# Kernel optimization log

Hardware: AMD Instinct MI355X
Metric: run time of the kernel (lower is better)

## Reference

```python
import jax, jax.numpy as jnp
import numpy as np

# Irreps config: node = 64x0e + 32x1o, edge sh = 1x0e + 1x1o
N, E = 50000, 800000
MUL0, MUL1 = 64, 32
D_IN = MUL0 + 3 * MUL1          # 160
FC_H = 64
W_NUMEL = MUL0 + MUL0 + MUL1 + MUL1  # 192, per-instruction uvu weights
SQRT3 = 1.7320508075688772
ACT_C = 1.6791   # e3nn normalize2mom constant for silu


def setup_inputs() -> dict:
    key = jax.random.key(0)
    ks = jax.random.split(key, 11)
    return {
        "x": jax.random.normal(ks[0], (N, D_IN), jnp.float32),
        "edge_scalars": jax.random.uniform(ks[1], (E, FC_H), dtype=jnp.float32),
        "edge_attr_sh": jax.random.normal(ks[2], (E, 4), jnp.float32),
        "edge_index": jax.random.randint(ks[3], (2, E), 0, N),
        "w_fc1": jax.random.normal(ks[4], (FC_H, FC_H), jnp.float32),
        "w_fc2": jax.random.normal(ks[5], (FC_H, W_NUMEL), jnp.float32),
        "w_sc_s": jax.random.normal(ks[6], (MUL0, MUL0), jnp.float32),
        "w_sc_v": jax.random.normal(ks[7], (MUL1, MUL1), jnp.float32),
        "w_lin_s": jax.random.normal(ks[8], (96, MUL0), jnp.float32),
        "w_lin_v": jax.random.normal(ks[9], (96, MUL1), jnp.float32),
        "w_alpha": jax.random.normal(ks[10], (96, 1), jnp.float32) * 0.1,
    }


def reference(x, edge_scalars, edge_attr_sh, edge_index, w_fc1, w_fc2,
              w_sc_s, w_sc_v, w_lin_s, w_lin_v, w_alpha):
    src, dst = edge_index[0], edge_index[1]

    # --- fc: FullyConnectedNet([64, 64, 192], silu), e3nn fan-in norm ---
    h = jax.nn.silu(edge_scalars @ w_fc1 / np.sqrt(FC_H)) * ACT_C
    weight = h @ w_fc2 / np.sqrt(FC_H)                       # [E, 192]
    w0 = weight[:, :MUL0]                 # 0e x 0e -> 0e (mul 64)
    w1 = weight[:, MUL0:2 * MUL0]         # 0e x 1o -> 1o (mul 64)
    w2 = weight[:, 2 * MUL0:2 * MUL0 + MUL1]   # 1o x 0e -> 1o (mul 32)
    w3 = weight[:, 2 * MUL0 + MUL1:]           # 1o x 1o -> 0e (mul 32)

    # --- self connection: o3.Linear(in -> out), per-irrep mixing ---
    x_s = x[:, :MUL0]                                   # [N, 64]
    x_v = x[:, MUL0:].reshape(N, MUL1, 3)               # [N, 32, 3]
    sc_s = x_s @ w_sc_s / np.sqrt(MUL0)
    sc_v = jnp.einsum('nui,uw->nwi', x_v, w_sc_v) / np.sqrt(MUL1)
    sc_out = jnp.concatenate([sc_s, sc_v.reshape(N, 3 * MUL1)], axis=1)

    # --- gather + edge-weighted uvu tensor product ---
    gx_s = x_s[src]                                     # [E, 64]
    gx_v = x_v[src]                                     # [E, 32, 3]
    sh_s = edge_attr_sh[:, 0:1]                         # [E, 1]
    sh_v = edge_attr_sh[:, 1:4]                         # [E, 3]

    # path weights fold with w3j so factors cancel for 1o outputs
    mid_s0 = w0 * gx_s * sh_s                                        # [E,64] 0e
    mid_s1 = w3 * jnp.einsum('eui,ei->eu', gx_v, sh_v) / SQRT3       # [E,32] 0e
    mid_v0 = w1[:, :, None] * gx_s[:, :, None] * sh_v[:, None, :]    # [E,64,3] 1o
    mid_v1 = w2[:, :, None] * gx_v * sh_s[:, :, None]                # [E,32,3] 1o
    edge_feat = jnp.concatenate(
        [mid_s0, mid_s1, mid_v0.reshape(E, 3 * MUL0), mid_v1.reshape(E, 3 * MUL1)],
        axis=1)                                                      # [E, 384]

    # --- scatter-mean to destination nodes ---
    seg = jax.ops.segment_sum(edge_feat, dst, num_segments=N)
    cnt = jax.ops.segment_sum(jnp.ones((E,), edge_feat.dtype), dst, num_segments=N)
    mean = seg / jnp.maximum(cnt, 1.0)[:, None]                      # [N, 384]

    m_s = mean[:, :96]                                   # 96x0e
    m_v = mean[:, 96:].reshape(N, 96, 3)                 # 96x1o

    # --- alpha gate (o3.Linear mid -> 0e) and output linear ---
    alpha = m_s @ w_alpha / np.sqrt(96)                  # [N, 1]
    lin_s = m_s @ w_lin_s / np.sqrt(96)                  # [N, 64]
    lin_v = jnp.einsum('nui,uw->nwi', m_v, w_lin_v) / np.sqrt(96)
    lin_out = jnp.concatenate([lin_s, lin_v.reshape(N, 3 * MUL1)], axis=1)

    # sc.output_mask is all-ones here (every output irrep reachable)
    return sc_out + alpha * lin_out
```

## Files before the change

kernel.cpp:

```cpp
#include <hip/hip_runtime.h>
#include <hip/hip_bf16.h>

#define N_NODES 50000
#define N_EDGES 800000
#define MUL0 64
#define MUL1 32
#define D_IN 160
#define FC_H 64
#define W_NUMEL 192
#define FEAT 384
#define ACT_C 1.6791f
#define INV_SQRT3 0.57735026918962576f
#define RSQRT32 0.17677669529663687f
#define RSQRT96 0.10206207261596575f

#define TILE 64
#define NWG_EDGE (N_EDGES / TILE)

typedef __attribute__((ext_vector_type(8))) short s16x8;
typedef __attribute__((ext_vector_type(4))) float f32x4;
typedef _Float16 h8 __attribute__((ext_vector_type(8)));
typedef __fp16 fp16x2 __attribute__((ext_vector_type(2)));

static __device__ __forceinline__ unsigned short f2bf(float f) {
    __hip_bfloat16 b = __float2bfloat16(f);
    return __builtin_bit_cast(unsigned short, b);
}

static __device__ __forceinline__ int swz(int row, int byte_in_row) {
    int unit = ((row & 1) << 2) | (byte_in_row >> 4);
    int su = unit ^ ((row >> 1) & 7);
    return (row >> 1) * 128 + su * 16 + (byte_in_row & 15);
}
static __device__ __forceinline__ h8 rdh8(const unsigned char* base, int row, int eb) {
    return *(const h8*)(base + swz(row, eb));
}


#define HIST_NB ((N_EDGES + 255) / 256)

__global__ __launch_bounds__(256) void hist_prep_kernel(
    const int*   __restrict__ eidx,
    int*         __restrict__ cnt,
    const float* __restrict__ w_fc1,
    const float* __restrict__ w_fc2,
    const float* __restrict__ w_sc_s,
    const float* __restrict__ w_sc_v,
    const float* __restrict__ w_lin_s,
    const float* __restrict__ w_lin_v,
    unsigned short* __restrict__ w1t,
    unsigned short* __restrict__ w2t,
    unsigned short* __restrict__ wscs_t,
    unsigned short* __restrict__ wscv_t,
    unsigned short* __restrict__ wlins_t,
    unsigned short* __restrict__ wlinv_t)
{
    int b = blockIdx.x;
    if (b < HIST_NB) {
        int e = b * 256 + threadIdx.x;
        if (e < N_EDGES) atomicAdd(&cnt[eidx[N_EDGES + e]], 1);
    } else {
        int i = (b - HIST_NB) * 256 + threadIdx.x;
        if (i < 64 * 64)  w1t[i]    = f2bf(w_fc1[(i & 63) * FC_H + (i >> 6)]);
        if (i < 192 * 64) w2t[i]    = f2bf(w_fc2[(i & 63) * W_NUMEL + (i >> 6)]);
        if (i < 64 * 64)  wscs_t[i] = f2bf(w_sc_s[(i & 63) * 64 + (i >> 6)]);
        if (i < 32 * 32)  wscv_t[i] = f2bf(w_sc_v[(i & 31) * 32 + (i >> 5)]);
        if (i < 64 * 96)  wlins_t[i] = f2bf(w_lin_s[(i % 96) * 64 + (i / 96)]);
        if (i < 32 * 96)  wlinv_t[i] = f2bf(w_lin_v[(i % 96) * 32 + (i / 96)]);
    }
}

#define SCAN_NB 64
#define SCAN_CH ((N_NODES + SCAN_NB - 1) / SCAN_NB)

__global__ __launch_bounds__(256) void scanA_kernel(const int* __restrict__ cnt,
                                                    int* __restrict__ bsum) {
    __shared__ int sred[4];
    int b = blockIdx.x, t = threadIdx.x;
    int lim = min((b + 1) * SCAN_CH, N_NODES);
    int s = 0;
    for (int i = b * SCAN_CH + t; i < lim; i += 256) s += cnt[i];
    for (int d = 1; d < 64; d <<= 1) s += __shfl_xor(s, d);
    if ((t & 63) == 0) sred[t >> 6] = s;
    __syncthreads();
    if (t == 0) bsum[b] = sred[0] + sred[1] + sred[2] + sred[3];
}

__global__ __launch_bounds__(256) void scanC_kernel(const int* __restrict__ cnt,
                                                    const int* __restrict__ bsum,
                                                    int* __restrict__ fill) {
    __shared__ int s_w[4];
    __shared__ int s_boff;
    int b = blockIdx.x, t = threadIdx.x;
    if (t < 64) {
        int v = bsum[t];
        int p = v;
        for (int d = 1; d < 64; d <<= 1) { int u = __shfl_up(p, d); if (t >= d) p += u; }
        if (t == b) s_boff = p - v;
    }
    const int CH2 = (SCAN_CH + 255) / 256;
    int base = b * SCAN_CH + t * CH2;
    int lim = min((b + 1) * SCAN_CH, N_NODES);
    int s = 0;
#pragma unroll
    for (int k = 0; k < CH2; ++k) { int i = base + k; if (i < lim) s += cnt[i]; }
    int v = s;
    for (int d = 1; d < 64; d <<= 1) { int u = __shfl_up(v, d); if ((t & 63) >= d) v += u; }
    if ((t & 63) == 63) s_w[t >> 6] = v;
    __syncthreads();
    if (t == 0) { int run = 0; for (int w = 0; w < 4; ++w) { int tv = s_w[w]; s_w[w] = run; run += tv; } }
    __syncthreads();
    int run = s_boff + s_w[t >> 6] + (v - s);
#pragma unroll
    for (int k = 0; k < CH2; ++k) {
        int i = base + k;
        if (i < lim) { fill[i] = run; run += cnt[i]; }
    }
}

__global__ __launch_bounds__(256) void scatter_ids_kernel(const int* __restrict__ eidx,
                                                          int* __restrict__ fill,
                                                          int* __restrict__ sorted_eid,
                                                          int* __restrict__ sorted_src,
                                                          int* __restrict__ sorted_dst) {
    int e = blockIdx.x * 256 + threadIdx.x;
    if (e < N_EDGES) {
        int d = eidx[N_EDGES + e];
        int s = eidx[e];
        int p = atomicAdd(&fill[d], 1);
        sorted_eid[p] = e;
        sorted_src[p] = s;
        sorted_dst[p] = d;
    }
}

#define X_OFF    0
#define W_OFF    20480
#define SH_OFF   45056
#define SID_OFF  45568
#define SEGN_OFF 45696
#define NSEG_OFF 45952
#define SMEM_SZ  45968

static __device__ __forceinline__ h8 seg_mask(const unsigned* vv, unsigned tgt) {
    h8 a;
#pragma unroll
    for (int w2 = 0; w2 < 4; ++w2) {
        a[w2 * 2]     = ((vv[w2] & 0xffffu) == tgt) ? (_Float16)1.f : (_Float16)0.f;
        a[w2 * 2 + 1] = ((vv[w2] >> 16)     == tgt) ? (_Float16)1.f : (_Float16)0.f;
    }
    return a;
}

__global__ __launch_bounds__(256) void edge_kernel(
    const float* __restrict__ x,
    const float* __restrict__ es,
    const float* __restrict__ sh,
    const int*   __restrict__ sorted_eid,
    const int*   __restrict__ sorted_src,
    const int*   __restrict__ sorted_dst,
    const unsigned short* __restrict__ w1t,
    const unsigned short* __restrict__ w2t,
    float* __restrict__ accg)
{
    __shared__ __align__(16) unsigned char smem[SMEM_SZ];
    int* s_segnode = (int*)(smem + SEGN_OFF);
    unsigned short* s_sid = (unsigned short*)(smem + SID_OFF);

    const int t = threadIdx.x;
    const int l = t & 63;
    const int wv = t >> 6;
    const int lr = l & 15;
    const int lk = l >> 4;
    int bid;
    {
        const int nwg = NWG_EDGE;
        int orig = blockIdx.x;
        int xcd = orig & 7, idx = orig >> 3;
        int q = nwg >> 3, r = nwg & 7;
        bid = (xcd < r ? xcd * (q + 1) : r * (q + 1) + (xcd - r) * q) + idx;
    }
    const int tile0 = bid * TILE;

    int eid_own = sorted_eid[tile0 + wv * 16 + lr];
    float4 esf[4];
    {
        const float4* ep = (const float4*)(es + (size_t)eid_own * FC_H);
        esf[0] = ep[lk * 2];     esf[1] = ep[lk * 2 + 1];
        esf[2] = ep[8 + lk * 2]; esf[3] = ep[8 + lk * 2 + 1];
    }
    const int hs   = t >> 7;
    const int tt_h = t & 127;
    const int xe   = tt_h & 31;
    const int cgrp = tt_h >> 5;
    float4 xg[10];
    {
        const float4* xp = (const float4*)(x + (size_t)sorted_src[tile0 + hs * 32 + xe] * D_IN);
#pragma unroll
        for (int k = 0; k < 10; ++k) xg[k] = xp[cgrp * 10 + k];
    }
    float shv = sh[(size_t)sorted_eid[tile0 + (t >> 2)] * 4 + (t & 3)];
    if (wv == 0) {
        int dl = sorted_dst[tile0 + l];
        int nd = __shfl_down(dl, 1);
        bool flag = (l == 63) || (dl != nd);
        unsigned long long m = __ballot(flag);
        int sid = __popcll(m & ((1ull << l) - 1ull));
        s_sid[l] = (unsigned short)sid;
        if (flag) s_segnode[sid] = dl;
        if (l == 63) *(int*)(smem + NSEG_OFF) = sid + 1;
    }

    unsigned short* s_h = (unsigned short*)(smem + X_OFF);
    s16x8 afrag[2];
    {
        s16x8 a;
        a[0] = f2bf(esf[0].x); a[1] = f2bf(esf[0].y); a[2] = f2bf(esf[0].z); a[3] = f2bf(esf[0].w);
        a[4] = f2bf(esf[1].x); a[5] = f2bf(esf[1].y); a[6] = f2bf(esf[1].z); a[7] = f2bf(esf[1].w);
        afrag[0] = a;
        a[0] = f2bf(esf[2].x); a[1] = f2bf(esf[2].y); a[2] = f2bf(esf[2].z); a[3] = f2bf(esf[2].w);
        a[4] = f2bf(esf[3].x); a[5] = f2bf(esf[3].y); a[6] = f2bf(esf[3].z); a[7] = f2bf(esf[3].w);
        afrag[1] = a;
    }
#pragma unroll
    for (int nt = 0; nt < 4; ++nt) {
        f32x4 hacc = {0.f, 0.f, 0.f, 0.f};
#pragma unroll
        for (int kk = 0; kk < 2; ++kk) {
            s16x8 b = *(const s16x8*)(w1t + (nt * 16 + lr) * 64 + kk * 32 + lk * 8);
            hacc = __builtin_amdgcn_mfma_f32_16x16x32_bf16(afrag[kk], b, hacc, 0, 0, 0);
        }
#pragma unroll
        for (int q = 0; q < 4; ++q) {
            float aa = hacc[q] * 0.125f;
            float hv = aa * (1.f / (1.f + __expf(-aa))) * ACT_C;
            s_h[(wv * 16 + lk * 4 + q) * 72 + nt * 16 + lr] = f2bf(hv);
        }
    }
    s16x8 hfrag[2];
#pragma unroll
    for (int kk = 0; kk < 2; ++kk)
        hfrag[kk] = *(const s16x8*)(s_h + (wv * 16 + lr) * 72 + kk * 32 + lk * 8);
    __syncthreads();

    {
        const int ws = wv >> 1;
        const int ebyte = (wv & 1) * 32 + lk * 8;
        unsigned char* bw = smem + W_OFF + ws * 12288;
#pragma unroll
        for (int nt = 0; nt < 12; ++nt) {
            f32x4 acc = {0.f, 0.f, 0.f, 0.f};
#pragma unroll
            for (int kk = 0; kk < 2; ++kk) {
                s16x8 b = *(const s16x8*)(w2t + (nt * 16 + lr) * 64 + kk * 32 + lk * 8);
                acc = __builtin_amdgcn_mfma_f32_16x16x32_bf16(hfrag[kk], b, acc, 0, 0, 0);
            }
            int f = nt * 16 + lr;
            fp16x2 p0 = __builtin_amdgcn_cvt_pkrtz(acc[0] * 0.125f, acc[1] * 0.125f);
            fp16x2 p1 = __builtin_amdgcn_cvt_pkrtz(acc[2] * 0.125f, acc[3] * 0.125f);
            uint2 wval = { __builtin_bit_cast(unsigned, p0), __builtin_bit_cast(unsigned, p1) };
            *(uint2*)(bw + swz(f, ebyte)) = wval;
        }
    }
    {
        unsigned char* bx = smem + X_OFF + hs * 10240;
#pragma unroll
        for (int k = 0; k < 10; ++k) {
            float4 v = xg[k];
#pragma unroll
            for (int jj = 0; jj < 4; ++jj) {
                int r = (cgrp * 10 + k) * 4 + jj;
                float fv = (jj == 0) ? v.x : (jj == 1) ? v.y : (jj == 2) ? v.z : v.w;
                *(_Float16*)(bx + swz(r, xe * 2)) = (_Float16)fv;
            }
        }
    }
    {
        int e = t >> 2, c = t & 3;
        *(_Float16*)(smem + SH_OFF + (e >> 5) * 256 + swz(c, (e & 31) * 2)) = (_Float16)shv;
    }
    __syncthreads();

    const int nseg = *(const int*)(smem + NSEG_OFF);
    const int eb = lk * 16;

    h8 shreg[4][2];
    unsigned vv[2][4];
#pragma unroll
    for (int ks = 0; ks < 2; ++ks) {
#pragma unroll
        for (int r = 0; r < 4; ++r)
            shreg[r][ks] = rdh8(smem + SH_OFF + ks * 256, r, eb);
        uint4 sv = *(const uint4*)(smem + SID_OFF + ks * 64 + lk * 16);
        vv[ks][0] = sv.x; vv[ks][1] = sv.y; vv[ks][2] = sv.z; vv[ks][3] = sv.w;
    }

    h8 Bv[4][2];
    int fcol[4];
    bool cls3j[4] = {false, false, false, false};
#pragma unroll
    for (int ks = 0; ks < 2; ++ks) {
        const unsigned char* bx = smem + X_OFF + ks * 10240;
        const unsigned char* bw = smem + W_OFF + ks * 12288;
        if (wv == 0) {
#pragma unroll
            for (int jj = 0; jj < 4; ++jj) {
                int col = jj * 16 + lr;
                Bv[jj][ks] = rdh8(bw, col, eb) * rdh8(bx, col, eb);
                fcol[jj] = col;
            }
        } else if (wv == 1) {
#pragma unroll
            for (int jj = 0; jj < 4; ++jj) {
                int col = jj * 16 + lr;
                Bv[jj][ks] = rdh8(bw, 128 + col / 3, eb) * rdh8(bx, 64 + col, eb);
                fcol[jj] = 288 + col;
            }
        } else if (wv == 2) {
#pragma unroll
            for (int jj = 0; jj < 2; ++jj) {
                int col = 64 + jj * 16 + lr;
                Bv[jj][ks] = rdh8(bw, 128 + col / 3, eb) * rdh8(bx, 64 + col, eb);
                fcol[jj] = 288 + col;
            }
#pragma unroll
            for (int jj = 2; jj < 4; ++jj) {
                int col = (jj - 2) * 16 + lr;
                h8 d = rdh8(bx, 64 + 3 * col, eb)     * shreg[1][ks]
                     + rdh8(bx, 64 + 3 * col + 1, eb) * shreg[2][ks]
                     + rdh8(bx, 64 + 3 * col + 2, eb) * shreg[3][ks];
                Bv[jj][ks] = rdh8(bw, 160 + col, eb) * d;
                fcol[jj] = 64 + col;
                cls3j[jj] = true;
            }
        } else {
#pragma unroll
            for (int jj = 0; jj < 4; ++jj) {
                int col = jj * 16 + lr;
                Bv[jj][ks] = rdh8(bw, 64 + col, eb) * rdh8(bx, col, eb);
                fcol[jj] = 96 + 3 * col;
            }
        }
    }

    if (wv != 3) {
        const int npass = (nseg + 15) >> 4;
        for (int p = 0; p < npass; ++p) {
            h8 bm0 = seg_mask(vv[0], (unsigned)(p * 16 + lr));
            h8 bm1 = seg_mask(vv[1], (unsigned)(p * 16 + lr));
            h8 As0 = bm0 * shreg[0][0];
            h8 As1 = bm1 * shreg[0][1];
            const int m0 = p * 16 + lk * 4;
            float* nptr[4]; bool valid[4], atq[4];
#pragma unroll
            for (int q = 0; q < 4; ++q) {
                int sg = m0 + q;
                valid[q] = sg < nseg;
                int node = valid[q] ? s_segnode[sg] : 0;
                nptr[q] = accg + (size_t)node * FEAT;
                atq[q] = (sg == 0) || (sg == nseg - 1);
            }
#pragma unroll
            for (int jj = 0; jj < 4; ++jj) {
                f32x4 acc = {0.f, 0.f, 0.f, 0.f};
                acc = __builtin_amdgcn_mfma_f32_16x16x32_f16(cls3j[jj] ? bm0 : As0, Bv[jj][0], acc, 0, 0, 0);
                acc = __builtin_amdgcn_mfma_f32_16x16x32_f16(cls3j[jj] ? bm1 : As1, Bv[jj][1], acc, 0, 0, 0);
                const float sc = cls3j[jj] ? INV_SQRT3 : 1.f;
#pragma unroll
                for (int q = 0; q < 4; ++q) {
                    if (valid[q]) {
                        float v = acc[q] * sc;
                        float* a = nptr[q] + fcol[jj];
                        if (atq[q]) atomicAdd(a, v); else *a = v;
                    }
                }
            }
        }
    } else {
        const int npass = (3 * nseg + 15) >> 4;
        for (int p = 0; p < npass; ++p) {
            int m = p * 16 + lr;
            int sgA = m / 3, i3A = m - 3 * sgA;
            h8 mk0 = seg_mask(vv[0], (unsigned)sgA);
            h8 mk1 = seg_mask(vv[1], (unsigned)sgA);
            h8 A0 = mk0 * ((i3A == 0) ? shreg[1][0] : (i3A == 1) ? shreg[2][0] : shreg[3][0]);
            h8 A1 = mk1 * ((i3A == 0) ? shreg[1][1] : (i3A == 1) ? shreg[2][1] : shreg[3][1]);
            int m0 = p * 16 + lk * 4;
            int sgq = m0 / 3, rq = m0 - 3 * sgq;
            float* nptr[4]; int i3q[4]; bool valid[4], atq[4];
#pragma unroll
            for (int q = 0; q < 4; ++q) {
                valid[q] = sgq < nseg;
                int node = valid[q] ? s_segnode[sgq] : 0;
                nptr[q] = accg + (size_t)node * FEAT;
                i3q[q] = rq;
                atq[q] = (sgq == 0) || (sgq == nseg - 1);
                if (++rq == 3) { rq = 0; ++sgq; }
            }
#pragma unroll
            for (int jj = 0; jj < 4; ++jj) {
                f32x4 acc = {0.f, 0.f, 0.f, 0.f};
                acc = __builtin_amdgcn_mfma_f32_16x16x32_f16(A0, Bv[jj][0], acc, 0, 0, 0);
                acc = __builtin_amdgcn_mfma_f32_16x16x32_f16(A1, Bv[jj][1], acc, 0, 0, 0);
#pragma unroll
                for (int q = 0; q < 4; ++q) {
                    if (valid[q]) {
                        float* a = nptr[q] + fcol[jj] + i3q[q];
                        if (atq[q]) atomicAdd(a, acc[q]); else *a = acc[q];
                    }
                }
            }
        }
    }
}


static __device__ __forceinline__ s16x8 frag_c8(const float* p, float s) {
    float4 u = *(const float4*)p, v = *(const float4*)(p + 4);
    s16x8 a;
    a[0] = f2bf(u.x * s); a[1] = f2bf(u.y * s); a[2] = f2bf(u.z * s); a[3] = f2bf(u.w * s);
    a[4] = f2bf(v.x * s); a[5] = f2bf(v.y * s); a[6] = f2bf(v.z * s); a[7] = f2bf(v.w * s);
    return a;
}

__global__ __launch_bounds__(256) void node_kernel(
    const float* __restrict__ x,
    const float* __restrict__ accg,
    const int*   __restrict__ cnt,
    const unsigned short* __restrict__ wscs_t,
    const unsigned short* __restrict__ wscv_t,
    const unsigned short* __restrict__ wlins_t,
    const unsigned short* __restrict__ wlinv_t,
    const float* __restrict__ w_alpha,
    float* __restrict__ out)
{
    const int t = threadIdx.x;
    const int wv = t >> 6, l = t & 63;
    const int lr = l & 15, lk = l >> 4;
    const int n_base = blockIdx.x * 64 + wv * 16;
    const int nrow = n_base + lr;
    const int nclamp = min(nrow, N_NODES - 1);

    const float* mrow = accg + (size_t)nclamp * FEAT;
    const float* xrow = x + (size_t)nclamp * D_IN;
    const float rinv = 1.f / (float)max(cnt[nclamp], 1);

    s16x8 ax[2], ams[3], axv[3], amv[3][3];
#pragma unroll
    for (int kk = 0; kk < 2; ++kk) ax[kk] = frag_c8(xrow + kk * 32 + lk * 8, 1.f);
#pragma unroll
    for (int kk = 0; kk < 3; ++kk) ams[kk] = frag_c8(mrow + kk * 32 + lk * 8, rinv);
    {
        float xb[24];
        const float4* p = (const float4*)(xrow + 64 + 24 * lk);
#pragma unroll
        for (int q = 0; q < 6; ++q) ((float4*)xb)[q] = p[q];
#pragma unroll
        for (int i = 0; i < 3; ++i) {
            s16x8 a;
#pragma unroll
            for (int j = 0; j < 8; ++j) a[j] = f2bf(xb[3 * j + i]);
            axv[i] = a;
        }
    }
#pragma unroll
    for (int kk = 0; kk < 3; ++kk) {
        float mb[24];
        const float4* p = (const float4*)(mrow + 96 + 96 * kk + 24 * lk);
#pragma unroll
        for (int q = 0; q < 6; ++q) ((float4*)mb)[q] = p[q];
#pragma unroll
        for (int i = 0; i < 3; ++i) {
            s16x8 a;
#pragma unroll
            for (int j = 0; j < 8; ++j) a[j] = f2bf(mb[3 * j + i] * rinv);
            amv[i][kk] = a;
        }
    }

    float ap = 0.f;
    {
        float ab[24];
        const float4* p = (const float4*)(mrow + 24 * lk);
#pragma unroll
        for (int q = 0; q < 6; ++q) ((float4*)ab)[q] = p[q];
#pragma unroll
        for (int j = 0; j < 24; ++j) ap += ab[j] * rinv * w_alpha[lk * 24 + j];
    }
    ap += __shfl_xor(ap, 16);
    ap += __shfl_xor(ap, 32);
    const float alphav = ap * RSQRT96;

    f32x4 accA[4], accL[4];
#pragma unroll
    for (int nt = 0; nt < 4; ++nt) { accA[nt] = (f32x4){0,0,0,0}; accL[nt] = (f32x4){0,0,0,0}; }
#pragma unroll
    for (int nt = 0; nt < 4; ++nt) {
#pragma unroll
        for (int kk = 0; kk < 2; ++kk) {
            s16x8 b = *(const s16x8*)(wscs_t + (nt * 16 + lr) * 64 + kk * 32 + lk * 8);
            accA[nt] = __builtin_amdgcn_mfma_f32_16x16x32_bf16(ax[kk], b, accA[nt], 0, 0, 0);
        }
#pragma unroll
        for (int kk = 0; kk < 3; ++kk) {
            s16x8 b = *(const s16x8*)(wlins_t + (nt * 16 + lr) * 96 + kk * 32 + lk * 8);
            accL[nt] = __builtin_amdgcn_mfma_f32_16x16x32_bf16(ams[kk], b, accL[nt], 0, 0, 0);
        }
    }
    f32x4 accVs[3][2], accVl[3][2];
#pragma unroll
    for (int i = 0; i < 3; ++i)
#pragma unroll
        for (int nt = 0; nt < 2; ++nt) { accVs[i][nt] = (f32x4){0,0,0,0}; accVl[i][nt] = (f32x4){0,0,0,0}; }
#pragma unroll
    for (int i = 0; i < 3; ++i) {
#pragma unroll
        for (int nt = 0; nt < 2; ++nt) {
            s16x8 b = *(const s16x8*)(wscv_t + (nt * 16 + lr) * 32 + lk * 8);
            accVs[i][nt] = __builtin_amdgcn_mfma_f32_16x16x32_bf16(axv[i], b, accVs[i][nt], 0, 0, 0);
#pragma unroll
            for (int kk = 0; kk < 3; ++kk) {
                s16x8 b2 = *(const s16x8*)(wlinv_t + (nt * 16 + lr) * 96 + kk * 32 + lk * 8);
                accVl[i][nt] = __builtin_amdgcn_mfma_f32_16x16x32_bf16(amv[i][kk], b2, accVl[i][nt], 0, 0, 0);
            }
        }
    }

#pragma unroll
    for (int q = 0; q < 4; ++q) {
        int row = lk * 4 + q;
        float ar = __shfl(alphav, row);
        int n = n_base + row;
        bool ok = (n < N_NODES);
        float* orow = out + (size_t)n * 160;
#pragma unroll
        for (int nt = 0; nt < 4; ++nt) {
            float vout = accA[nt][q] * 0.125f + ar * accL[nt][q] * RSQRT96;
            if (ok) orow[nt * 16 + lr] = vout;
        }
#pragma unroll
        for (int i = 0; i < 3; ++i)
#pragma unroll
            for (int nt = 0; nt < 2; ++nt) {
                float vout = accVs[i][nt][q] * RSQRT32 + ar * accVl[i][nt][q] * RSQRT96;
                if (ok) orow[64 + 3 * (nt * 16 + lr) + i] = vout;
            }
    }
}


extern "C" void kernel_launch(void* const* d_in, const int* in_sizes, int n_in,
                              void* d_out, int out_size, void* d_ws, size_t ws_size,
                              hipStream_t stream) {
    const float* x        = (const float*)d_in[0];
    const float* es       = (const float*)d_in[1];
    const float* sh       = (const float*)d_in[2];
    const int*   eidx     = (const int*)d_in[3];
    const float* w_fc1    = (const float*)d_in[4];
    const float* w_fc2    = (const float*)d_in[5];
    const float* w_sc_s   = (const float*)d_in[6];
    const float* w_sc_v   = (const float*)d_in[7];
    const float* w_lin_s  = (const float*)d_in[8];
    const float* w_lin_v  = (const float*)d_in[9];
    const float* w_alpha  = (const float*)d_in[10];
    float* out = (float*)d_out;

    float* accg       = (float*)d_ws;
    int*   cnt        = (int*)(accg + (size_t)N_NODES * FEAT);
    int*   fill       = cnt + N_NODES;
    int*   sorted_eid = fill + N_NODES;
    int*   sorted_src = sorted_eid + N_EDGES;
    int*   sorted_dst = sorted_src + N_EDGES;
    unsigned short* w1t     = (unsigned short*)(sorted_dst + N_EDGES);
    unsigned short* w2t     = w1t + 64 * 64;
    unsigned short* wscs_t  = w2t + 192 * 64;
    unsigned short* wscv_t  = wscs_t + 64 * 64;
    unsigned short* wlins_t = wscv_t + 32 * 32;
    unsigned short* wlinv_t = wlins_t + 64 * 96;
    int* bsum = (int*)(wlinv_t + 32 * 96);

    (void)hipMemsetAsync(d_ws, 0, ((size_t)N_NODES * FEAT + N_NODES) * 4, stream);
    hipLaunchKernelGGL(hist_prep_kernel, dim3(HIST_NB + 48), dim3(256), 0, stream,
                       eidx, cnt, w_fc1, w_fc2, w_sc_s, w_sc_v, w_lin_s, w_lin_v,
                       w1t, w2t, wscs_t, wscv_t, wlins_t, wlinv_t);
    hipLaunchKernelGGL(scanA_kernel, dim3(SCAN_NB), dim3(256), 0, stream, cnt, bsum);
    hipLaunchKernelGGL(scanC_kernel, dim3(SCAN_NB), dim3(256), 0, stream, cnt, bsum, fill);
    hipLaunchKernelGGL(scatter_ids_kernel, dim3((N_EDGES + 255) / 256), dim3(256), 0, stream,
                       eidx, fill, sorted_eid, sorted_src, sorted_dst);
    hipLaunchKernelGGL(edge_kernel, dim3(NWG_EDGE), dim3(256), 0, stream,
                       x, es, sh, sorted_eid, sorted_src, sorted_dst, w1t, w2t, accg);
    hipLaunchKernelGGL(node_kernel, dim3((N_NODES + 63) / 64), dim3(256), 0, stream,
                       x, accg, cnt, wscs_t, wscv_t, wlins_t, wlinv_t, w_alpha, out);
}
```

Baseline: 453.5 us.

## Split fused edge kernel into MLP weight kernel and scatter kernel

Measured after the change: 548.1 us. +20.9%, slower.

```diff
diff --git a/kernel.cpp b/kernel.cpp
--- a/kernel.cpp
+++ b/kernel.cpp
@@ -16,11 +16,14 @@
 
 #define TILE 64
 #define NWG_EDGE (N_EDGES / TILE)
+#define WT_TILE_BYTES 24576
 
 typedef __attribute__((ext_vector_type(8))) short s16x8;
 typedef __attribute__((ext_vector_type(4))) float f32x4;
 typedef _Float16 h8 __attribute__((ext_vector_type(8)));
 typedef __fp16 fp16x2 __attribute__((ext_vector_type(2)));
+typedef __attribute__((address_space(1))) const void gv_t;
+typedef __attribute__((address_space(3))) void lv_t;
 
 static __device__ __forceinline__ unsigned short f2bf(float f) {
     __hip_bfloat16 b = __float2bfloat16(f);
@@ -134,6 +137,79 @@
     }
 }
 
+
+__global__ __launch_bounds__(256) void mlp_kernel(
+    const float* __restrict__ es,
+    const int*   __restrict__ sorted_eid,
+    const unsigned short* __restrict__ w1t,
+    const unsigned short* __restrict__ w2t,
+    unsigned char* __restrict__ wsT)
+{
+    __shared__ unsigned short s_h[64 * 72];
+
+    const int t = threadIdx.x;
+    const int l = t & 63;
+    const int wv = t >> 6;
+    const int lr = l & 15;
+    const int lk = l >> 4;
+    const int tile0 = blockIdx.x * TILE;
+
+    int eid_own = sorted_eid[tile0 + wv * 16 + lr];
+    float4 esf[4];
+    {
+        const float4* ep = (const float4*)(es + (size_t)eid_own * FC_H);
+        esf[0] = ep[lk * 2];     esf[1] = ep[lk * 2 + 1];
+        esf[2] = ep[8 + lk * 2]; esf[3] = ep[8 + lk * 2 + 1];
+    }
+
+    s16x8 afrag[2];
+    {
+        s16x8 a;
+        a[0] = f2bf(esf[0].x); a[1] = f2bf(esf[0].y); a[2] = f2bf(esf[0].z); a[3] = f2bf(esf[0].w);
+        a[4] = f2bf(esf[1].x); a[5] = f2bf(esf[1].y); a[6] = f2bf(esf[1].z); a[7] = f2bf(esf[1].w);
+        afrag[0] = a;
+        a[0] = f2bf(esf[2].x); a[1] = f2bf(esf[2].y); a[2] = f2bf(esf[2].z); a[3] = f2bf(esf[2].w);
+        a[4] = f2bf(esf[3].x); a[5] = f2bf(esf[3].y); a[6] = f2bf(esf[3].z); a[7] = f2bf(esf[3].w);
+        afrag[1] = a;
+    }
+#pragma unroll
+    for (int nt = 0; nt < 4; ++nt) {
+        f32x4 hacc = {0.f, 0.f, 0.f, 0.f};
+#pragma unroll
+        for (int kk = 0; kk < 2; ++kk) {
+            s16x8 b = *(const s16x8*)(w1t + (nt * 16 + lr) * 64 + kk * 32 + lk * 8);
+            hacc = __builtin_amdgcn_mfma_f32_16x16x32_bf16(afrag[kk], b, hacc, 0, 0, 0);
+        }
+#pragma unroll
+        for (int q = 0; q < 4; ++q) {
+            float aa = hacc[q] * 0.125f;
+            float hv = aa * (1.f / (1.f + __expf(-aa))) * ACT_C;
+            s_h[(wv * 16 + lk * 4 + q) * 72 + nt * 16 + lr] = f2bf(hv);
+        }
+    }
+    s16x8 hfrag[2];
+#pragma unroll
+    for (int kk = 0; kk < 2; ++kk)
+        hfrag[kk] = *(const s16x8*)(s_h + (wv * 16 + lr) * 72 + kk * 32 + lk * 8);
+
+    unsigned char* bw = wsT + (size_t)blockIdx.x * WT_TILE_BYTES + (wv >> 1) * 12288;
+    const int ebyte = (wv & 1) * 32 + lk * 8;
+#pragma unroll
+    for (int nt = 0; nt < 12; ++nt) {
+        f32x4 acc = {0.f, 0.f, 0.f, 0.f};
+#pragma unroll
+        for (int kk = 0; kk < 2; ++kk) {
+            s16x8 b = *(const s16x8*)(w2t + (nt * 16 + lr) * 64 + kk * 32 + lk * 8);
+            acc = __builtin_amdgcn_mfma_f32_16x16x32_bf16(hfrag[kk], b, acc, 0, 0, 0);
+        }
+        int f = nt * 16 + lr;
+        fp16x2 p0 = __builtin_amdgcn_cvt_pkrtz(acc[0] * 0.125f, acc[1] * 0.125f);
+        fp16x2 p1 = __builtin_amdgcn_cvt_pkrtz(acc[2] * 0.125f, acc[3] * 0.125f);
+        uint2 wval = { __builtin_bit_cast(unsigned, p0), __builtin_bit_cast(unsigned, p1) };
+        *(uint2*)(bw + swz(f, ebyte)) = wval;
+    }
+}
+
 #define X_OFF    0
 #define W_OFF    20480
 #define SH_OFF   45056
@@ -151,6 +227,227 @@
     }
     return a;
 }
+
+static __device__ __forceinline__ void phase_c(
+    unsigned char* smem, int wv, int lr, int lk, float* __restrict__ accg)
+{
+    int* s_segnode = (int*)(smem + SEGN_OFF);
+    const int nseg = *(const int*)(smem + NSEG_OFF);
+    const int eb = lk * 16;
+
+    h8 shreg[4][2];
+    unsigned vv[2][4];
+#pragma unroll
+    for (int ks = 0; ks < 2; ++ks) {
+#pragma unroll
+        for (int r = 0; r < 4; ++r)
+            shreg[r][ks] = rdh8(smem + SH_OFF + ks * 256, r, eb);
+        uint4 sv = *(const uint4*)(smem + SID_OFF + ks * 64 + lk * 16);
+        vv[ks][0] = sv.x; vv[ks][1] = sv.y; vv[ks][2] = sv.z; vv[ks][3] = sv.w;
+    }
+
+    h8 Bv[4][2];
+    int fcol[4];
+    bool cls3j[4] = {false, false, false, false};
+#pragma unroll
+    for (int ks = 0; ks < 2; ++ks) {
+        const unsigned char* bx = smem + X_OFF + ks * 10240;
+        const unsigned char* bw = smem + W_OFF + ks * 12288;
+        if (wv == 0) {
+#pragma unroll
+            for (int jj = 0; jj < 4; ++jj) {
+                int col = jj * 16 + lr;
+                Bv[jj][ks] = rdh8(bw, col, eb) * rdh8(bx, col, eb);
+                fcol[jj] = col;
+            }
+        } else if (wv == 1) {
+#pragma unroll
+            for (int jj = 0; jj < 4; ++jj) {
+                int col = jj * 16 + lr;
+                Bv[jj][ks] = rdh8(bw, 128 + col / 3, eb) * rdh8(bx, 64 + col, eb);
+                fcol[jj] = 288 + col;
+            }
+        } else if (wv == 2) {
+#pragma unroll
+            for (int jj = 0; jj < 2; ++jj) {
+                int col = 64 + jj * 16 + lr;
+                Bv[jj][ks] = rdh8(bw, 128 + col / 3, eb) * rdh8(bx, 64 + col, eb);
+                fcol[jj] = 288 + col;
+            }
+#pragma unroll
+            for (int jj = 2; jj < 4; ++jj) {
+                int col = (jj - 2) * 16 + lr;
+                h8 d = rdh8(bx, 64 + 3 * col, eb)     * shreg[1][ks]
+                     + rdh8(bx, 64 + 3 * col + 1, eb) * shreg[2][ks]
+                     + rdh8(bx, 64 + 3 * col + 2, eb) * shreg[3][ks];
+                Bv[jj][ks] = rdh8(bw, 160 + col, eb) * d;
+                fcol[jj] = 64 + col;
+                cls3j[jj] = true;
+            }
+        } else {
+#pragma unroll
+            for (int jj = 0; jj < 4; ++jj) {
+                int col = jj * 16 + lr;
+                Bv[jj][ks] = rdh8(bw, 64 + col, eb) * rdh8(bx, col, eb);
+                fcol[jj] = 96 + 3 * col;
+            }
+        }
+    }
+
+    if (wv != 3) {
+        const int npass = (nseg + 15) >> 4;
+        for (int p = 0; p < npass; ++p) {
+            h8 bm0 = seg_mask(vv[0], (unsigned)(p * 16 + lr));
+            h8 bm1 = seg_mask(vv[1], (unsigned)(p * 16 + lr));
+            h8 As0 = bm0 * shreg[0][0];
+            h8 As1 = bm1 * shreg[0][1];
+            const int m0 = p * 16 + lk * 4;
+            float* nptr[4]; bool valid[4], atq[4];
+#pragma unroll
+            for (int q = 0; q < 4; ++q) {
+                int sg = m0 + q;
+                valid[q] = sg < nseg;
+                int node = valid[q] ? s_segnode[sg] : 0;
+                nptr[q] = accg + (size_t)node * FEAT;
+                atq[q] = (sg == 0) || (sg == nseg - 1);
+            }
+#pragma unroll
+            for (int jj = 0; jj < 4; ++jj) {
+                f32x4 acc = {0.f, 0.f, 0.f, 0.f};
+                acc = __builtin_amdgcn_mfma_f32_16x16x32_f16(cls3j[jj] ? bm0 : As0, Bv[jj][0], acc, 0, 0, 0);
+                acc = __builtin_amdgcn_mfma_f32_16x16x32_f16(cls3j[jj] ? bm1 : As1, Bv[jj][1], acc, 0, 0, 0);
+                const float sc = cls3j[jj] ? INV_SQRT3 : 1.f;
+#pragma unroll
+                for (int q = 0; q < 4; ++q) {
+                    if (valid[q]) {
+                        float v = acc[q] * sc;
+                        float* a = nptr[q] + fcol[jj];
+                        if (atq[q]) atomicAdd(a, v); else *a = v;
+                    }
+                }
+            }
+        }
+    } else {
+        const int npass = (3 * nseg + 15) >> 4;
+        for (int p = 0; p < npass; ++p) {
+            int m = p * 16 + lr;
+            int sgA = m / 3, i3A = m - 3 * sgA;
+            h8 mk0 = seg_mask(vv[0], (unsigned)sgA);
+            h8 mk1 = seg_mask(vv[1], (unsigned)sgA);
+            h8 A0 = mk0 * ((i3A == 0) ? shreg[1][0] : (i3A == 1) ? shreg[2][0] : shreg[3][0]);
+            h8 A1 = mk1 * ((i3A == 0) ? shreg[1][1] : (i3A == 1) ? shreg[2][1] : shreg[3][1]);
+            int m0 = p * 16 + lk * 4;
+            int sgq = m0 / 3, rq = m0 - 3 * sgq;
+            float* nptr[4]; int i3q[4]; bool valid[4], atq[4];
+#pragma unroll
+            for (int q = 0; q < 4; ++q) {
+                valid[q] = sgq < nseg;
+                int node = valid[q] ? s_segnode[sgq] : 0;
+                nptr[q] = accg + (size_t)node * FEAT;
+                i3q[q] = rq;
+                atq[q] = (sgq == 0) || (sgq == nseg - 1);
+                if (++rq == 3) { rq = 0; ++sgq; }
+            }
+#pragma unroll
+            for (int jj = 0; jj < 4; ++jj) {
+                f32x4 acc = {0.f, 0.f, 0.f, 0.f};
+                acc = __builtin_amdgcn_mfma_f32_16x16x32_f16(A0, Bv[jj][0], acc, 0, 0, 0);
+                acc = __builtin_amdgcn_mfma_f32_16x16x32_f16(A1, Bv[jj][1], acc, 0, 0, 0);
+#pragma unroll
+                for (int q = 0; q < 4; ++q) {
+                    if (valid[q]) {
+                        float* a = nptr[q] + fcol[jj] + i3q[q];
+                        if (atq[q]) atomicAdd(a, acc[q]); else *a = acc[q];
+                    }
+                }
+            }
+        }
+    }
+}
+
+
+__global__ __launch_bounds__(256) void scatter_kernel(
+    const float* __restrict__ x,
+    const float* __restrict__ sh,
+    const int*   __restrict__ sorted_eid,
+    const int*   __restrict__ sorted_src,
+    const int*   __restrict__ sorted_dst,
+    const unsigned char* __restrict__ wsT,
+    float* __restrict__ accg)
+{
+    __shared__ __align__(16) unsigned char smem[SMEM_SZ];
+    int* s_segnode = (int*)(smem + SEGN_OFF);
+    unsigned short* s_sid = (unsigned short*)(smem + SID_OFF);
+
+    const int t = threadIdx.x;
+    const int l = t & 63;
+    const int wv = t >> 6;
+    const int lr = l & 15;
+    const int lk = l >> 4;
+    int bid;
+    {
+        const int nwg = NWG_EDGE;
+        int orig = blockIdx.x;
+        int xcd = orig & 7, idx = orig >> 3;
+        int q = nwg >> 3, r = nwg & 7;
+        bid = (xcd < r ? xcd * (q + 1) : r * (q + 1) + (xcd - r) * q) + idx;
+    }
+    const int tile0 = bid * TILE;
+
+    {
+        const unsigned char* gsrc = wsT + (size_t)bid * WT_TILE_BYTES;
+#pragma unroll
+        for (int i = 0; i < 6; ++i) {
+            __builtin_amdgcn_global_load_lds(
+                (gv_t*)(gsrc + i * 4096 + wv * 1024 + l * 16),
+                (lv_t*)(smem + W_OFF + i * 4096 + wv * 1024), 16, 0, 0);
+        }
+    }
+
+    const int hs   = t >> 7;
+    const int tt_h = t & 127;
+    const int xe   = tt_h & 31;
+    const int cgrp = tt_h >> 5;
+    float4 xg[10];
+    {
+        const float4* xp = (const float4*)(x + (size_t)sorted_src[tile0 + hs * 32 + xe] * D_IN);
+#pragma unroll
+        for (int k = 0; k < 10; ++k) xg[k] = xp[cgrp * 10 + k];
+    }
+    float shv = sh[(size_t)sorted_eid[tile0 + (t >> 2)] * 4 + (t & 3)];
+    if (wv == 0) {
+        int dl = sorted_dst[tile0 + l];
+        int nd = __shfl_down(dl, 1);
+        bool flag = (l == 63) || (dl != nd);
+        unsigned long long m = __ballot(flag);
+        int sid = __popcll(m & ((1ull << l) - 1ull));
+        s_sid[l] = (unsigned short)sid;
+        if (flag) s_segnode[sid] = dl;
+        if (l == 63) *(int*)(smem + NSEG_OFF) = sid + 1;
+    }
+
+    {
+        unsigned char* bx = smem + X_OFF + hs * 10240;
+#pragma unroll
+        for (int k = 0; k < 10; ++k) {
+            float4 v = xg[k];
+#pragma unroll
+            for (int jj = 0; jj < 4; ++jj) {
+                int r = (cgrp * 10 + k) * 4 + jj;
+                float fv = (jj == 0) ? v.x : (jj == 1) ? v.y : (jj == 2) ? v.z : v.w;
+                *(_Float16*)(bx + swz(r, xe * 2)) = (_Float16)fv;
+            }
+        }
+    }
+    {
+        int e = t >> 2, c = t & 3;
+        *(_Float16*)(smem + SH_OFF + (e >> 5) * 256 + swz(c, (e & 31) * 2)) = (_Float16)shv;
+    }
+    __syncthreads();
+
+    phase_c(smem, wv, lr, lk, accg);
+}
+
 
 __global__ __launch_bounds__(256) void edge_kernel(
     const float* __restrict__ x,
@@ -281,137 +578,7 @@
     }
     __syncthreads();
 
-    const int nseg = *(const int*)(smem + NSEG_OFF);
-    const int eb = lk * 16;
-
-    h8 shreg[4][2];
-    unsigned vv[2][4];
-#pragma unroll
-    for (int ks = 0; ks < 2; ++ks) {
-#pragma unroll
-        for (int r = 0; r < 4; ++r)
-            shreg[r][ks] = rdh8(smem + SH_OFF + ks * 256, r, eb);
-        uint4 sv = *(const uint4*)(smem + SID_OFF + ks * 64 + lk * 16);
-        vv[ks][0] = sv.x; vv[ks][1] = sv.y; vv[ks][2] = sv.z; vv[ks][3] = sv.w;
-    }
-
-    h8 Bv[4][2];
-    int fcol[4];
-    bool cls3j[4] = {false, false, false, false};
-#pragma unroll
-    for (int ks = 0; ks < 2; ++ks) {
-        const unsigned char* bx = smem + X_OFF + ks * 10240;
-        const unsigned char* bw = smem + W_OFF + ks * 12288;
-        if (wv == 0) {
-#pragma unroll
-            for (int jj = 0; jj < 4; ++jj) {
-                int col = jj * 16 + lr;
-                Bv[jj][ks] = rdh8(bw, col, eb) * rdh8(bx, col, eb);
-                fcol[jj] = col;
-            }
-        } else if (wv == 1) {
-#pragma unroll
-            for (int jj = 0; jj < 4; ++jj) {
-                int col = jj * 16 + lr;
-                Bv[jj][ks] = rdh8(bw, 128 + col / 3, eb) * rdh8(bx, 64 + col, eb);
-                fcol[jj] = 288 + col;
-            }
-        } else if (wv == 2) {
-#pragma unroll
-            for (int jj = 0; jj < 2; ++jj) {
-                int col = 64 + jj * 16 + lr;
-                Bv[jj][ks] = rdh8(bw, 128 + col / 3, eb) * rdh8(bx, 64 + col, eb);
-                fcol[jj] = 288 + col;
-            }
-#pragma unroll
-            for (int jj = 2; jj < 4; ++jj) {
-                int col = (jj - 2) * 16 + lr;
-                h8 d = rdh8(bx, 64 + 3 * col, eb)     * shreg[1][ks]
-                     + rdh8(bx, 64 + 3 * col + 1, eb) * shreg[2][ks]
-                     + rdh8(bx, 64 + 3 * col + 2, eb) * shreg[3][ks];
-                Bv[jj][ks] = rdh8(bw, 160 + col, eb) * d;
-                fcol[jj] = 64 + col;
-                cls3j[jj] = true;
-            }
-        } else {
-#pragma unroll
-            for (int jj = 0; jj < 4; ++jj) {
-                int col = jj * 16 + lr;
-                Bv[jj][ks] = rdh8(bw, 64 + col, eb) * rdh8(bx, col, eb);
-                fcol[jj] = 96 + 3 * col;
-            }
-        }
-    }
-
-    if (wv != 3) {
-        const int npass = (nseg + 15) >> 4;
-        for (int p = 0; p < npass; ++p) {
-            h8 bm0 = seg_mask(vv[0], (unsigned)(p * 16 + lr));
-            h8 bm1 = seg_mask(vv[1], (unsigned)(p * 16 + lr));
-            h8 As0 = bm0 * shreg[0][0];
-            h8 As1 = bm1 * shreg[0][1];
-            const int m0 = p * 16 + lk * 4;
-            float* nptr[4]; bool valid[4], atq[4];
-#pragma unroll
-            for (int q = 0; q < 4; ++q) {
-                int sg = m0 + q;
-                valid[q] = sg < nseg;
-                int node = valid[q] ? s_segnode[sg] : 0;
-                nptr[q] = accg + (size_t)node * FEAT;
-                atq[q] = (sg == 0) || (sg == nseg - 1);
-            }
-#pragma unroll
-            for (int jj = 0; jj < 4; ++jj) {
-                f32x4 acc = {0.f, 0.f, 0.f, 0.f};
-                acc = __builtin_amdgcn_mfma_f32_16x16x32_f16(cls3j[jj] ? bm0 : As0, Bv[jj][0], acc, 0, 0, 0);
-                acc = __builtin_amdgcn_mfma_f32_16x16x32_f16(cls3j[jj] ? bm1 : As1, Bv[jj][1], acc, 0, 0, 0);
-                const float sc = cls3j[jj] ? INV_SQRT3 : 1.f;
-#pragma unroll
-                for (int q = 0; q < 4; ++q) {
-                    if (valid[q]) {
-                        float v = acc[q] * sc;
-                        float* a = nptr[q] + fcol[jj];
-                        if (atq[q]) atomicAdd(a, v); else *a = v;
-                    }
-                }
-            }
-        }
-    } else {
-        const int npass = (3 * nseg + 15) >> 4;
-        for (int p = 0; p < npass; ++p) {
-            int m = p * 16 + lr;
-            int sgA = m / 3, i3A = m - 3 * sgA;
-            h8 mk0 = seg_mask(vv[0], (unsigned)sgA);
-            h8 mk1 = seg_mask(vv[1], (unsigned)sgA);
-            h8 A0 = mk0 * ((i3A == 0) ? shreg[1][0] : (i3A == 1) ? shreg[2][0] : shreg[3][0]);
-            h8 A1 = mk1 * ((i3A == 0) ? shreg[1][1] : (i3A == 1) ? shreg[2][1] : shreg[3][1]);
-            int m0 = p * 16 + lk * 4;
-            int sgq = m0 / 3, rq = m0 - 3 * sgq;
-            float* nptr[4]; int i3q[4]; bool valid[4], atq[4];
-#pragma unroll
-            for (int q = 0; q < 4; ++q) {
-                valid[q] = sgq < nseg;
-                int node = valid[q] ? s_segnode[sgq] : 0;
-                nptr[q] = accg + (size_t)node * FEAT;
-                i3q[q] = rq;
-                atq[q] = (sgq == 0) || (sgq == nseg - 1);
-                if (++rq == 3) { rq = 0; ++sgq; }
-            }
-#pragma unroll
-            for (int jj = 0; jj < 4; ++jj) {
-                f32x4 acc = {0.f, 0.f, 0.f, 0.f};
-                acc = __builtin_amdgcn_mfma_f32_16x16x32_f16(A0, Bv[jj][0], acc, 0, 0, 0);
-                acc = __builtin_amdgcn_mfma_f32_16x16x32_f16(A1, Bv[jj][1], acc, 0, 0, 0);
-#pragma unroll
-                for (int q = 0; q < 4; ++q) {
-                    if (valid[q]) {
-                        float* a = nptr[q] + fcol[jj] + i3q[q];
-                        if (atq[q]) atomicAdd(a, acc[q]); else *a = acc[q];
-                    }
-                }
-            }
-        }
-    }
+    phase_c(smem, wv, lr, lk, accg);
 }
 
 
@@ -578,6 +745,11 @@
     unsigned short* wlins_t = wscv_t + 32 * 32;
     unsigned short* wlinv_t = wlins_t + 64 * 96;
     int* bsum = (int*)(wlinv_t + 32 * 96);
+    size_t base_bytes = (size_t)((unsigned char*)(bsum + SCAN_NB) - (unsigned char*)d_ws);
+    base_bytes = (base_bytes + 15) & ~(size_t)15;
+    unsigned char* wsT = (unsigned char*)d_ws + base_bytes;
+    size_t needed = base_bytes + (size_t)NWG_EDGE * WT_TILE_BYTES;
+    const bool use_split = (ws_size >= needed);
 
     (void)hipMemsetAsync(d_ws, 0, ((size_t)N_NODES * FEAT + N_NODES) * 4, stream);
     hipLaunchKernelGGL(hist_prep_kernel, dim3(HIST_NB + 48), dim3(256), 0, stream,
@@ -587,8 +759,15 @@
     hipLaunchKernelGGL(scanC_kernel, dim3(SCAN_NB), dim3(256), 0, stream, cnt, bsum, fill);
     hipLaunchKernelGGL(scatter_ids_kernel, dim3((N_EDGES + 255) / 256), dim3(256), 0, stream,
                        eidx, fill, sorted_eid, sorted_src, sorted_dst);
-    hipLaunchKernelGGL(edge_kernel, dim3(NWG_EDGE), dim3(256), 0, stream,
-                       x, es, sh, sorted_eid, sorted_src, sorted_dst, w1t, w2t, accg);
+    if (use_split) {
+        hipLaunchKernelGGL(mlp_kernel, dim3(NWG_EDGE), dim3(256), 0, stream,
+                           es, sorted_eid, w1t, w2t, wsT);
+        hipLaunchKernelGGL(scatter_kernel, dim3(NWG_EDGE), dim3(256), 0, stream,
+                           x, sh, sorted_eid, sorted_src, sorted_dst, wsT, accg);
+    } else {
+        hipLaunchKernelGGL(edge_kernel, dim3(NWG_EDGE), dim3(256), 0, stream,
+                           x, es, sh, sorted_eid, sorted_src, sorted_dst, w1t, w2t, accg);
+    }
     hipLaunchKernelGGL(node_kernel, dim3((N_NODES + 63) / 64), dim3(256), 0, stream,
                        x, accg, cnt, wscs_t, wscv_t, wlins_t, wlinv_t, w_alpha, out);
 }
```

## Pre-permute edge scalars to bf16 and sh into sorted order during scatter

Applied to the files above, without the earlier changes.

New measurement: 517.7 us. +14.1%, slower.

```diff
diff --git a/kernel.cpp b/kernel.cpp
--- a/kernel.cpp
+++ b/kernel.cpp
@@ -118,19 +118,32 @@
     }
 }
 
-__global__ __launch_bounds__(256) void scatter_ids_kernel(const int* __restrict__ eidx,
-                                                          int* __restrict__ fill,
-                                                          int* __restrict__ sorted_eid,
-                                                          int* __restrict__ sorted_src,
-                                                          int* __restrict__ sorted_dst) {
+__global__ __launch_bounds__(256) void scatter_ids_kernel(
+    const int*   __restrict__ eidx,
+    const float* __restrict__ es,
+    const float* __restrict__ sh,
+    int* __restrict__ fill,
+    int* __restrict__ sorted_src,
+    int* __restrict__ sorted_dst,
+    unsigned short* __restrict__ es16s,
+    float* __restrict__ shs)
+{
     int e = blockIdx.x * 256 + threadIdx.x;
     if (e < N_EDGES) {
         int d = eidx[N_EDGES + e];
         int s = eidx[e];
         int p = atomicAdd(&fill[d], 1);
-        sorted_eid[p] = e;
         sorted_src[p] = s;
         sorted_dst[p] = d;
+        const float4* srcp = (const float4*)(es + (size_t)e * FC_H);
+        ushort4* dstp = (ushort4*)(es16s + (size_t)p * FC_H);
+#pragma unroll
+        for (int k = 0; k < 16; ++k) {
+            float4 v = srcp[k];
+            ushort4 u = { f2bf(v.x), f2bf(v.y), f2bf(v.z), f2bf(v.w) };
+            dstp[k] = u;
+        }
+        *(float4*)(shs + (size_t)p * 4) = *(const float4*)(sh + (size_t)e * 4);
     }
 }
 
@@ -154,9 +167,8 @@
 
 __global__ __launch_bounds__(256) void edge_kernel(
     const float* __restrict__ x,
-    const float* __restrict__ es,
-    const float* __restrict__ sh,
-    const int*   __restrict__ sorted_eid,
+    const unsigned short* __restrict__ es16s,
+    const float* __restrict__ shs,
     const int*   __restrict__ sorted_src,
     const int*   __restrict__ sorted_dst,
     const unsigned short* __restrict__ w1t,
@@ -182,12 +194,11 @@
     }
     const int tile0 = bid * TILE;
 
-    int eid_own = sorted_eid[tile0 + wv * 16 + lr];
-    float4 esf[4];
-    {
-        const float4* ep = (const float4*)(es + (size_t)eid_own * FC_H);
-        esf[0] = ep[lk * 2];     esf[1] = ep[lk * 2 + 1];
-        esf[2] = ep[8 + lk * 2]; esf[3] = ep[8 + lk * 2 + 1];
+    s16x8 afrag[2];
+    {
+        const unsigned short* ep = es16s + (size_t)(tile0 + wv * 16 + lr) * FC_H;
+        afrag[0] = *(const s16x8*)(ep + lk * 8);
+        afrag[1] = *(const s16x8*)(ep + 32 + lk * 8);
     }
     const int hs   = t >> 7;
     const int tt_h = t & 127;
@@ -199,7 +210,7 @@
 #pragma unroll
         for (int k = 0; k < 10; ++k) xg[k] = xp[cgrp * 10 + k];
     }
-    float shv = sh[(size_t)sorted_eid[tile0 + (t >> 2)] * 4 + (t & 3)];
+    float shv = shs[(size_t)tile0 * 4 + t];
     if (wv == 0) {
         int dl = sorted_dst[tile0 + l];
         int nd = __shfl_down(dl, 1);
@@ -212,16 +223,6 @@
     }
 
     unsigned short* s_h = (unsigned short*)(smem + X_OFF);
-    s16x8 afrag[2];
-    {
-        s16x8 a;
-        a[0] = f2bf(esf[0].x); a[1] = f2bf(esf[0].y); a[2] = f2bf(esf[0].z); a[3] = f2bf(esf[0].w);
-        a[4] = f2bf(esf[1].x); a[5] = f2bf(esf[1].y); a[6] = f2bf(esf[1].z); a[7] = f2bf(esf[1].w);
-        afrag[0] = a;
-        a[0] = f2bf(esf[2].x); a[1] = f2bf(esf[2].y); a[2] = f2bf(esf[2].z); a[3] = f2bf(esf[2].w);
-        a[4] = f2bf(esf[3].x); a[5] = f2bf(esf[3].y); a[6] = f2bf(esf[3].z); a[7] = f2bf(esf[3].w);
-        afrag[1] = a;
-    }
 #pragma unroll
     for (int nt = 0; nt < 4; ++nt) {
         f32x4 hacc = {0.f, 0.f, 0.f, 0.f};
@@ -568,8 +569,7 @@
     float* accg       = (float*)d_ws;
     int*   cnt        = (int*)(accg + (size_t)N_NODES * FEAT);
     int*   fill       = cnt + N_NODES;
-    int*   sorted_eid = fill + N_NODES;
-    int*   sorted_src = sorted_eid + N_EDGES;
+    int*   sorted_src = fill + N_NODES;
     int*   sorted_dst = sorted_src + N_EDGES;
     unsigned short* w1t     = (unsigned short*)(sorted_dst + N_EDGES);
     unsigned short* w2t     = w1t + 64 * 64;
@@ -578,6 +578,10 @@
     unsigned short* wlins_t = wscv_t + 32 * 32;
     unsigned short* wlinv_t = wlins_t + 64 * 96;
     int* bsum = (int*)(wlinv_t + 32 * 96);
+    size_t base_bytes = (size_t)((unsigned char*)(bsum + SCAN_NB) - (unsigned char*)d_ws);
+    base_bytes = (base_bytes + 15) & ~(size_t)15;
+    unsigned short* es16s = (unsigned short*)((unsigned char*)d_ws + base_bytes);
+    float* shs = (float*)(es16s + (size_t)N_EDGES * FC_H);
 
     (void)hipMemsetAsync(d_ws, 0, ((size_t)N_NODES * FEAT + N_NODES) * 4, stream);
     hipLaunchKernelGGL(hist_prep_kernel, dim3(HIST_NB + 48), dim3(256), 0, stream,
@@ -586,9 +590,9 @@
     hipLaunchKernelGGL(scanA_kernel, dim3(SCAN_NB), dim3(256), 0, stream, cnt, bsum);
     hipLaunchKernelGGL(scanC_kernel, dim3(SCAN_NB), dim3(256), 0, stream, cnt, bsum, fill);
     hipLaunchKernelGGL(scatter_ids_kernel, dim3((N_EDGES + 255) / 256), dim3(256), 0, stream,
-                       eidx, fill, sorted_eid, sorted_src, sorted_dst);
+                       eidx, es, sh, fill, sorted_src, sorted_dst, es16s, shs);
     hipLaunchKernelGGL(edge_kernel, dim3(NWG_EDGE), dim3(256), 0, stream,
-                       x, es, sh, sorted_eid, sorted_src, sorted_dst, w1t, w2t, accg);
+                       x, es16s, shs, sorted_src, sorted_dst, w1t, w2t, accg);
     hipLaunchKernelGGL(node_kernel, dim3((N_NODES + 63) / 64), dim3(256), 0, stream,
                        x, accg, cnt, wscs_t, wscv_t, wlins_t, wlinv_t, w_alpha, out);
 }
```
